# Optimization experiments

Hardware: AMD Instinct MI355X
Metric: run time of the kernel (lower is better)

Reference implementation:

```python
import jax, jax.numpy as jnp
import numpy as np

H, KV, DH = 16, 4, 64  # num_heads, num_kv_heads, head_dim


def setup_inputs() -> dict:
    key = jax.random.key(0)
    k1, k2, k3, k4, k5 = jax.random.split(key, 5)
    B, L, D = 1, 4096, 1024
    s = 0.02
    return {
        "x": jax.random.normal(k1, (B, L, D), dtype=jnp.float32),
        "Wq": jax.random.normal(k2, (D, H * DH), dtype=jnp.float32) * s,
        "Wk": jax.random.normal(k3, (D, KV * DH), dtype=jnp.float32) * s,
        "Wv": jax.random.normal(k4, (D, KV * DH), dtype=jnp.float32) * s,
        "Wo": jax.random.normal(k5, (H * DH, D), dtype=jnp.float32) * s,
    }


def _rotate_half(t):
    t1, t2 = t[..., : DH // 2], t[..., DH // 2 :]
    return jnp.concatenate([-t2, t1], axis=-1)


def reference(x, Wq, Wk, Wv, Wo):
    B, L, D = x.shape
    G = H // KV  # query heads per kv head
    q = (x @ Wq).reshape(B, L, H, DH)
    k = (x @ Wk).reshape(B, L, KV, DH)
    v = (x @ Wv).reshape(B, L, KV, DH)

    # RoPE: inv_freq over even dims, angles duplicated across both halves
    inv_freq = 1.0 / (10000.0 ** (jnp.arange(0, DH, 2, dtype=jnp.float32) / DH))
    t = jnp.arange(L, dtype=jnp.float32)
    freqs = t[:, None] * inv_freq[None, :]                 # [L, DH/2]
    emb = jnp.concatenate([freqs, freqs], axis=-1)[None, :, None, :]  # [1,L,1,DH]
    cos, sin = jnp.cos(emb), jnp.sin(emb)
    q = q * cos + _rotate_half(q) * sin
    k = k * cos + _rotate_half(k) * sin

    # GQA: query head h attends with kv head h // G (repeat_interleave layout)
    qg = q.reshape(B, L, KV, G, DH)
    scale = DH ** -0.5
    attn = jnp.einsum("bqkgd,bskd->bkgqs", qg, k) * scale  # [B,KV,G,L,L]
    attn = jax.nn.softmax(attn, axis=-1)
    out = jnp.einsum("bkgqs,bskd->bqkgd", attn, v).reshape(B, L, H * DH)
    return out @ Wo
```

## Files before the change

kernel.cpp:

```cpp
#include <hip/hip_runtime.h>
#include <math.h>

#define L 4096
#define D 1024
#define H 16
#define KV 4
#define DH 64

typedef __attribute__((ext_vector_type(8))) short bf16x8;
typedef __attribute__((ext_vector_type(4))) float f32x4;

static __device__ __forceinline__ unsigned short f2bf(float f) {
    unsigned u = __float_as_uint(f);
    u = (u + 0x7FFF + ((u >> 16) & 1)) >> 16;
    return (unsigned short)u;
}

#define EXP2F(x) __builtin_amdgcn_exp2f(x)

#define GLD16(src, dst) \
    __builtin_amdgcn_global_load_lds((__attribute__((address_space(1))) void*)(src), \
                                     (__attribute__((address_space(3))) void*)(dst), 16, 0, 0)

__global__ __launch_bounds__(256) void prep_kernel(
        const float* __restrict__ x,  const float* __restrict__ Wq,
        const float* __restrict__ Wk, const float* __restrict__ Wv,
        const float* __restrict__ Wo,
        unsigned short* __restrict__ xb, unsigned short* __restrict__ WqkvT,
        unsigned short* __restrict__ WoT) {
    const int b = blockIdx.x, tid = threadIdx.x;
    if (b < 4096) {
        int i = (b * 256 + tid) * 4;
        float4 v = *(const float4*)&x[i];
        ushort4 o;
        o.x = f2bf(v.x); o.y = f2bf(v.y); o.z = f2bf(v.z); o.w = f2bf(v.w);
        *(ushort4*)&xb[i] = o;
        return;
    }
    __shared__ float t[32][33];
    const float* src; unsigned short* dst; int N, n0, k0;
    if (b < 5120)      { int tq = b - 4096; src = Wq; dst = WqkvT;                     N = 1024; n0 = (tq & 31) * 32; k0 = (tq >> 5) * 32; }
    else if (b < 5376) { int tq = b - 5120; src = Wk; dst = WqkvT + (size_t)1024*1024; N = 256;  n0 = (tq & 7)  * 32; k0 = (tq >> 3) * 32; }
    else if (b < 5632) { int tq = b - 5376; src = Wv; dst = WqkvT + (size_t)1280*1024; N = 256;  n0 = (tq & 7)  * 32; k0 = (tq >> 3) * 32; }
    else               { int tq = b - 5632; src = Wo; dst = WoT;                       N = 1024; n0 = (tq & 31) * 32; k0 = (tq >> 5) * 32; }
    const int tx = tid & 31, ty = tid >> 5;
    #pragma unroll
    for (int j = 0; j < 4; ++j)
        t[ty + 8 * j][tx] = src[(size_t)(k0 + ty + 8 * j) * N + n0 + tx];
    __syncthreads();
    #pragma unroll
    for (int j = 0; j < 4; ++j)
        dst[(size_t)(n0 + ty + 8 * j) * 1024 + k0 + tx] = f2bf(t[tx][ty + 8 * j]);
}

__global__ __launch_bounds__(256) void gemm_bf16(const unsigned short* __restrict__ A,
                                                 const unsigned short* __restrict__ BT,
                                                 float* __restrict__ C,
                                                 int M, int N, int K) {
    __shared__ unsigned short As[128 * 32];
    __shared__ unsigned short Bs[128 * 32];

    const int tid  = threadIdx.x;
    const int w    = tid >> 6;
    const int lane = tid & 63;
    const int c    = lane & 15;
    const int quad = lane >> 4;
    const int wy = w >> 1, wx = w & 1;
    const int row0 = blockIdx.y * 128;
    const int col0 = blockIdx.x * 128;

    const int ld_row = w * 16 + (lane >> 2);
    const int ld_col = (lane & 3) * 8;

    f32x4 acc[4][4];
    #pragma unroll
    for (int mt = 0; mt < 4; ++mt)
        #pragma unroll
        for (int nt = 0; nt < 4; ++nt)
            acc[mt][nt] = (f32x4){0.f, 0.f, 0.f, 0.f};

    for (int k0 = 0; k0 < K; k0 += 32) {
        __syncthreads();
        GLD16(&A [(size_t)(row0 + ld_row)      * K + k0 + ld_col], &As[w * 512]);
        GLD16(&A [(size_t)(row0 + ld_row + 64) * K + k0 + ld_col], &As[w * 512 + 2048]);
        GLD16(&BT[(size_t)(col0 + ld_row)      * K + k0 + ld_col], &Bs[w * 512]);
        GLD16(&BT[(size_t)(col0 + ld_row + 64) * K + k0 + ld_col], &Bs[w * 512 + 2048]);
        __syncthreads();

        bf16x8 af[4], bfr[4];
        #pragma unroll
        for (int mt = 0; mt < 4; ++mt)
            af[mt] = *(const bf16x8*)&As[(wy * 64 + mt * 16 + c) * 32 + quad * 8];
        #pragma unroll
        for (int nt = 0; nt < 4; ++nt)
            bfr[nt] = *(const bf16x8*)&Bs[(wx * 64 + nt * 16 + c) * 32 + quad * 8];

        #pragma unroll
        for (int mt = 0; mt < 4; ++mt)
            #pragma unroll
            for (int nt = 0; nt < 4; ++nt)
                acc[mt][nt] = __builtin_amdgcn_mfma_f32_16x16x32_bf16(af[mt], bfr[nt], acc[mt][nt], 0, 0, 0);
    }

    #pragma unroll
    for (int mt = 0; mt < 4; ++mt)
        #pragma unroll
        for (int nt = 0; nt < 4; ++nt)
            #pragma unroll
            for (int r = 0; r < 4; ++r)
                C[(size_t)(row0 + wy * 64 + mt * 16 + quad * 4 + r) * N
                  + col0 + wx * 64 + nt * 16 + c] = acc[mt][nt][r];
}

__global__ __launch_bounds__(256) void gemm_qkv_rope(
        const unsigned short* __restrict__ A,
        const unsigned short* __restrict__ BT,
        unsigned short* __restrict__ qb,
        unsigned short* __restrict__ kbuf,
        unsigned short* __restrict__ vbuf) {
    __shared__ unsigned short As[128 * 32];
    __shared__ unsigned short Bs[128 * 32];

    const int tid  = threadIdx.x;
    const int w    = tid >> 6;
    const int lane = tid & 63;
    const int c    = lane & 15;
    const int quad = lane >> 4;
    const int wy = w >> 1, wx = w & 1;
    const int row0 = blockIdx.y * 128;
    const int col0 = blockIdx.x * 128;

    const int ld_row = w * 16 + (lane >> 2);
    const int ld_col = (lane & 3) * 8;

    f32x4 acc[4][4];
    #pragma unroll
    for (int mt = 0; mt < 4; ++mt)
        #pragma unroll
        for (int nt = 0; nt < 4; ++nt)
            acc[mt][nt] = (f32x4){0.f, 0.f, 0.f, 0.f};

    for (int k0 = 0; k0 < 1024; k0 += 32) {
        __syncthreads();
        GLD16(&A [(size_t)(row0 + ld_row)      * 1024 + k0 + ld_col], &As[w * 512]);
        GLD16(&A [(size_t)(row0 + ld_row + 64) * 1024 + k0 + ld_col], &As[w * 512 + 2048]);
        GLD16(&BT[(size_t)(col0 + ld_row)      * 1024 + k0 + ld_col], &Bs[w * 512]);
        GLD16(&BT[(size_t)(col0 + ld_row + 64) * 1024 + k0 + ld_col], &Bs[w * 512 + 2048]);
        __syncthreads();

        bf16x8 af[4], bfr[4];
        #pragma unroll
        for (int mt = 0; mt < 4; ++mt)
            af[mt] = *(const bf16x8*)&As[(wy * 64 + mt * 16 + c) * 32 + quad * 8];
        #pragma unroll
        for (int nt = 0; nt < 4; ++nt)
            bfr[nt] = *(const bf16x8*)&Bs[(wx * 64 + nt * 16 + c) * 32 + quad * 8];

        #pragma unroll
        for (int mt = 0; mt < 4; ++mt)
            #pragma unroll
            for (int nt = 0; nt < 4; ++nt)
                acc[mt][nt] = __builtin_amdgcn_mfma_f32_16x16x32_bf16(af[mt], bfr[nt], acc[mt][nt], 0, 0, 0);
    }

    const int colb = col0 + wx * 64;
    if (colb < 1280) {
        unsigned short* dst; int hh, hstride; float scale;
        if (colb < 1024) { dst = qb;   hh = colb >> 6;          hstride = H;  scale = 0.18033688011112042f; }
        else             { dst = kbuf; hh = (colb - 1024) >> 6; hstride = KV; scale = 1.0f; }
        #pragma unroll
        for (int nt = 0; nt < 2; ++nt) {
            int d = nt * 16 + c;
            float invf = EXP2F((float)d * -0.4152410118609203f);
            #pragma unroll
            for (int mt = 0; mt < 4; ++mt)
                #pragma unroll
                for (int r = 0; r < 4; ++r) {
                    int l = row0 + wy * 64 + mt * 16 + quad * 4 + r;
                    float ang = (float)l * invf;
                    float sn = __sinf(ang), cs = __cosf(ang);
                    float x1 = acc[mt][nt][r], x2 = acc[mt][nt + 2][r];
                    dst[((size_t)l * hstride + hh) * DH + d]      = f2bf((x1 * cs - x2 * sn) * scale);
                    dst[((size_t)l * hstride + hh) * DH + d + 32] = f2bf((x2 * cs + x1 * sn) * scale);
                }
        }
    } else {
        int vh = (colb - 1280) >> 6;
        #pragma unroll
        for (int mt = 0; mt < 4; ++mt)
            #pragma unroll
            for (int nt = 0; nt < 4; ++nt)
                #pragma unroll
                for (int r = 0; r < 4; ++r) {
                    int l = row0 + wy * 64 + mt * 16 + quad * 4 + r;
                    vbuf[((size_t)l * KV + vh) * DH + nt * 16 + c] = f2bf(acc[mt][nt][r]);
                }
    }
}

__global__ __launch_bounds__(512, 2) void attn_mfma_kernel(
        const unsigned short* __restrict__ qb,
        const unsigned short* __restrict__ kb,
        const unsigned short* __restrict__ vb,
        unsigned short* __restrict__ ob) {
    __shared__ __align__(16) unsigned short Vt[2][2][64][64];
    __shared__ __align__(16) unsigned short Ps[8][64][64];

    const int tid  = threadIdx.x;
    const int w    = tid >> 6;
    const int lane = tid & 63;
    const int c    = lane & 15;
    const int quad = lane >> 4;
    const int g    = w >> 2;
    const int kv = blockIdx.y;
    const int h  = kv * 4 + (w & 3);
    const int q0 = blockIdx.x * 64;
    const int s_base = g * 2048;

    bf16x8 qfrag[4][2];
    #pragma unroll
    for (int qt = 0; qt < 4; ++qt)
        #pragma unroll
        for (int kt = 0; kt < 2; ++kt)
            qfrag[qt][kt] = *(const bf16x8*)&qb[((size_t)(q0 + qt * 16 + c) * H + h) * DH
                                                + kt * 32 + quad * 8];

    f32x4 oacc[4][4];
    f32x4 oones[4];
    #pragma unroll
    for (int qt = 0; qt < 4; ++qt) {
        oones[qt] = (f32x4){0.f, 0.f, 0.f, 0.f};
        #pragma unroll
        for (int dt = 0; dt < 4; ++dt)
            oacc[qt][dt] = (f32x4){0.f, 0.f, 0.f, 0.f};
    }
    const short one_bf = (short)0x3F80;
    const bf16x8 ones8 = {one_bf, one_bf, one_bf, one_bf, one_bf, one_bf, one_bf, one_bf};

    const int tid8 = tid & 255;
    const int sp = tid8 & 31, dc = tid8 >> 5;
    unsigned short* PsW = &Ps[w][0][0];
    const int xr = c & 7;

    int4 vreg0 = *(const int4*)&vb[((size_t)(s_base + 2 * sp)     * KV + kv) * DH + dc * 8];
    int4 vreg1 = *(const int4*)&vb[((size_t)(s_base + 2 * sp + 1) * KV + kv) * DH + dc * 8];
    bf16x8 kA[4][2], kB[4][2];
    #pragma unroll
    for (int mt = 0; mt < 4; ++mt)
        #pragma unroll
        for (int kt = 0; kt < 2; ++kt)
            kA[mt][kt] = *(const bf16x8*)&kb[((size_t)(s_base + mt * 16 + c) * KV + kv) * DH + kt * 32 + quad * 8];

    auto step = [&](int it, int buf, bf16x8 kc[4][2], bf16x8 kn[4][2]) {
        {
            const unsigned* pa = (const unsigned*)&vreg0;
            const unsigned* pb = (const unsigned*)&vreg1;
            #pragma unroll
            for (int t = 0; t < 4; ++t) {
                unsigned lo = __builtin_amdgcn_perm(pb[t], pa[t], 0x05040100u);
                unsigned hi = __builtin_amdgcn_perm(pb[t], pa[t], 0x07060302u);
                int dl = dc * 8 + 2 * t, dh = dl + 1;
                *(unsigned*)&Vt[g][buf][dl][(((sp >> 2) ^ (dl & 7)) << 3) + 2 * (sp & 3)] = lo;
                *(unsigned*)&Vt[g][buf][dh][(((sp >> 2) ^ (dh & 7)) << 3) + 2 * (sp & 3)] = hi;
            }
        }
        __syncthreads();

        int s1 = s_base + ((it + 1) & 31) * 64;
        vreg0 = *(const int4*)&vb[((size_t)(s1 + 2 * sp)     * KV + kv) * DH + dc * 8];
        vreg1 = *(const int4*)&vb[((size_t)(s1 + 2 * sp + 1) * KV + kv) * DH + dc * 8];
        #pragma unroll
        for (int mt = 0; mt < 4; ++mt)
            #pragma unroll
            for (int kt = 0; kt < 2; ++kt)
                kn[mt][kt] = *(const bf16x8*)&kb[((size_t)(s1 + mt * 16 + c) * KV + kv) * DH + kt * 32 + quad * 8];

        #pragma unroll
        for (int mt = 0; mt < 4; ++mt) {
            f32x4 st[4];
            #pragma unroll
            for (int qt = 0; qt < 4; ++qt) {
                f32x4 a = (f32x4){0.f, 0.f, 0.f, 0.f};
                a = __builtin_amdgcn_mfma_f32_16x16x32_bf16(kc[mt][0], qfrag[qt][0], a, 0, 0, 0);
                a = __builtin_amdgcn_mfma_f32_16x16x32_bf16(kc[mt][1], qfrag[qt][1], a, 0, 0, 0);
                st[qt] = a;
            }
            #pragma unroll
            for (int qt = 0; qt < 4; ++qt) {
                float p0 = EXP2F(st[qt][0]);
                float p1 = EXP2F(st[qt][1]);
                float p2 = EXP2F(st[qt][2]);
                float p3 = EXP2F(st[qt][3]);
                uint2 pk;
                pk.x = __builtin_amdgcn_perm(__float_as_uint(p1), __float_as_uint(p0), 0x07060302u);
                pk.y = __builtin_amdgcn_perm(__float_as_uint(p3), __float_as_uint(p2), 0x07060302u);
                *(uint2*)&PsW[(qt * 16 + c) * 64 + (((2 * mt + (quad >> 1)) ^ xr) << 3) + (quad & 1) * 4] = pk;
            }
        }

        bf16x8 pf[4][2];
        #pragma unroll
        for (int qt = 0; qt < 4; ++qt)
            #pragma unroll
            for (int kt = 0; kt < 2; ++kt)
                pf[qt][kt] = *(const bf16x8*)&PsW[(qt * 16 + c) * 64 + (((kt * 4 + quad) ^ xr) << 3)];

        #pragma unroll
        for (int dt = 0; dt < 4; ++dt) {
            bf16x8 vf0 = *(const bf16x8*)&Vt[g][buf][dt * 16 + c][((0 * 4 + quad) ^ xr) << 3];
            bf16x8 vf1 = *(const bf16x8*)&Vt[g][buf][dt * 16 + c][((1 * 4 + quad) ^ xr) << 3];
            #pragma unroll
            for (int qt = 0; qt < 4; ++qt) {
                oacc[qt][dt] = __builtin_amdgcn_mfma_f32_16x16x32_bf16(pf[qt][0], vf0, oacc[qt][dt], 0, 0, 0);
                oacc[qt][dt] = __builtin_amdgcn_mfma_f32_16x16x32_bf16(pf[qt][1], vf1, oacc[qt][dt], 0, 0, 0);
            }
        }
        #pragma unroll
        for (int qt = 0; qt < 4; ++qt) {
            oones[qt] = __builtin_amdgcn_mfma_f32_16x16x32_bf16(pf[qt][0], ones8, oones[qt], 0, 0, 0);
            oones[qt] = __builtin_amdgcn_mfma_f32_16x16x32_bf16(pf[qt][1], ones8, oones[qt], 0, 0, 0);
        }
    };

    for (int it = 0; it < 32; it += 2) {
        step(it,     0, kA, kB);
        step(it + 1, 1, kB, kA);
    }

    __syncthreads();
    if (g == 1) {
        float* dsto = (float*)&Ps[0][0][0] + (size_t)(w - 4) * 4096 + lane * 64;
        #pragma unroll
        for (int qt = 0; qt < 4; ++qt)
            #pragma unroll
            for (int dt = 0; dt < 4; ++dt)
                *(f32x4*)&dsto[qt * 16 + dt * 4] = oacc[qt][dt];
        float* dsts = (float*)&Vt[0][0][0][0] + (size_t)(w - 4) * 1024 + lane * 16;
        #pragma unroll
        for (int qt = 0; qt < 4; ++qt)
            *(f32x4*)&dsts[qt * 4] = oones[qt];
    }
    __syncthreads();
    if (g == 0) {
        const float* srco = (const float*)&Ps[0][0][0] + (size_t)w * 4096 + lane * 64;
        const float* srcs = (const float*)&Vt[0][0][0][0] + (size_t)w * 1024 + lane * 16;
        #pragma unroll
        for (int qt = 0; qt < 4; ++qt) {
            f32x4 po = *(const f32x4*)&srcs[qt * 4];
            oones[qt] += po;
            #pragma unroll
            for (int dt = 0; dt < 4; ++dt)
                oacc[qt][dt] += *(const f32x4*)&srco[qt * 16 + dt * 4];
        }
        #pragma unroll
        for (int qt = 0; qt < 4; ++qt)
            #pragma unroll
            for (int r = 0; r < 4; ++r) {
                float inv = 1.0f / oones[qt][r];
                int row = q0 + qt * 16 + quad * 4 + r;
                #pragma unroll
                for (int dt = 0; dt < 4; ++dt)
                    ob[(size_t)row * (H * DH) + h * DH + dt * 16 + c] = f2bf(oacc[qt][dt][r] * inv);
            }
    }
}

extern "C" void kernel_launch(void* const* d_in, const int* in_sizes, int n_in,
                              void* d_out, int out_size, void* d_ws, size_t ws_size,
                              hipStream_t stream) {
    const float* x  = (const float*)d_in[0];
    const float* Wq = (const float*)d_in[1];
    const float* Wk = (const float*)d_in[2];
    const float* Wv = (const float*)d_in[3];
    const float* Wo = (const float*)d_in[4];
    float* out = (float*)d_out;

    char* ws = (char*)d_ws;
    unsigned short* xb    = (unsigned short*)ws;
    unsigned short* ob    = xb;
    unsigned short* qb    = (unsigned short*)(ws + 8388608);
    unsigned short* kb    = (unsigned short*)(ws + 16777216);
    unsigned short* vb    = (unsigned short*)(ws + 18874368);
    unsigned short* WqkvT = (unsigned short*)(ws + 20971520);
    unsigned short* WoT   = (unsigned short*)(ws + 24117248);

    dim3 blk(256);

    prep_kernel<<<6656, blk, 0, stream>>>(x, Wq, Wk, Wv, Wo, xb, WqkvT, WoT);

    gemm_qkv_rope<<<dim3(12, 32), blk, 0, stream>>>(xb, WqkvT, qb, kb, vb);

    attn_mfma_kernel<<<dim3(L / 64, KV), dim3(512), 0, stream>>>(qb, kb, vb, ob);

    gemm_bf16<<<dim3(D / 128, L / 128), blk, 0, stream>>>(ob, WoT, out, L, D, D);
}
```

Baseline: 230.4 us.

## Store V transposed from QKV GEMM and load V fragments directly in attention

The QKV GEMM epilogue now writes V in a transposed [kv*64+d][L] layout with packed 8-byte stores. The attention kernel then loads V MFMA operands straight from global memory instead of staging and transposing V through LDS. This drops the per-iteration __syncthreads and the LDS V buffer, and shrinks shared memory to one buffer. The final cross-group reduction is redone in two halves through that smaller LDS region. The cost is more global and L2 traffic per wave, since each wave group reloads V with no sharing through LDS.

```diff
diff --git a/kernel.cpp b/kernel.cpp
--- a/kernel.cpp
+++ b/kernel.cpp
@@ -117,7 +117,7 @@
         const unsigned short* __restrict__ BT,
         unsigned short* __restrict__ qb,
         unsigned short* __restrict__ kbuf,
-        unsigned short* __restrict__ vbuf) {
+        unsigned short* __restrict__ vtb) {
     __shared__ unsigned short As[128 * 32];
     __shared__ unsigned short Bs[128 * 32];
 
@@ -187,24 +187,25 @@
     } else {
         int vh = (colb - 1280) >> 6;
         #pragma unroll
-        for (int mt = 0; mt < 4; ++mt)
-            #pragma unroll
-            for (int nt = 0; nt < 4; ++nt)
-                #pragma unroll
-                for (int r = 0; r < 4; ++r) {
-                    int l = row0 + wy * 64 + mt * 16 + quad * 4 + r;
-                    vbuf[((size_t)l * KV + vh) * DH + nt * 16 + c] = f2bf(acc[mt][nt][r]);
-                }
+        for (int mt = 0; mt < 4; ++mt) {
+            int l0 = row0 + wy * 64 + mt * 16 + quad * 4;
+            #pragma unroll
+            for (int nt = 0; nt < 4; ++nt) {
+                unsigned u0 = (unsigned)f2bf(acc[mt][nt][0]) | ((unsigned)f2bf(acc[mt][nt][1]) << 16);
+                unsigned u1 = (unsigned)f2bf(acc[mt][nt][2]) | ((unsigned)f2bf(acc[mt][nt][3]) << 16);
+                uint2 pk; pk.x = u0; pk.y = u1;
+                *(uint2*)&vtb[(size_t)((vh * 64 + nt * 16 + c) << 12) + l0] = pk;
+            }
+        }
     }
 }
 
 __global__ __launch_bounds__(512, 2) void attn_mfma_kernel(
         const unsigned short* __restrict__ qb,
         const unsigned short* __restrict__ kb,
-        const unsigned short* __restrict__ vb,
+        const unsigned short* __restrict__ vtb,
         unsigned short* __restrict__ ob) {
-    __shared__ __align__(16) unsigned short Vt[2][2][64][64];
-    __shared__ __align__(16) unsigned short Ps[8][64][64];
+    __shared__ __align__(16) unsigned short lds[32768];
 
     const int tid  = threadIdx.x;
     const int w    = tid >> 6;
@@ -237,13 +238,10 @@
     const short one_bf = (short)0x3F80;
     const bf16x8 ones8 = {one_bf, one_bf, one_bf, one_bf, one_bf, one_bf, one_bf, one_bf};
 
-    const int tid8 = tid & 255;
-    const int sp = tid8 & 31, dc = tid8 >> 5;
-    unsigned short* PsW = &Ps[w][0][0];
+    unsigned short* PsW = &lds[w * 4096];
     const int xr = c & 7;
-
-    int4 vreg0 = *(const int4*)&vb[((size_t)(s_base + 2 * sp)     * KV + kv) * DH + dc * 8];
-    int4 vreg1 = *(const int4*)&vb[((size_t)(s_base + 2 * sp + 1) * KV + kv) * DH + dc * 8];
+    const unsigned short* vrow = &vtb[(size_t)((kv * 64 + c) << 12)];
+
     bf16x8 kA[4][2], kB[4][2];
     #pragma unroll
     for (int mt = 0; mt < 4; ++mt)
@@ -251,24 +249,17 @@
         for (int kt = 0; kt < 2; ++kt)
             kA[mt][kt] = *(const bf16x8*)&kb[((size_t)(s_base + mt * 16 + c) * KV + kv) * DH + kt * 32 + quad * 8];
 
-    auto step = [&](int it, int buf, bf16x8 kc[4][2], bf16x8 kn[4][2]) {
-        {
-            const unsigned* pa = (const unsigned*)&vreg0;
-            const unsigned* pb = (const unsigned*)&vreg1;
-            #pragma unroll
-            for (int t = 0; t < 4; ++t) {
-                unsigned lo = __builtin_amdgcn_perm(pb[t], pa[t], 0x05040100u);
-                unsigned hi = __builtin_amdgcn_perm(pb[t], pa[t], 0x07060302u);
-                int dl = dc * 8 + 2 * t, dh = dl + 1;
-                *(unsigned*)&Vt[g][buf][dl][(((sp >> 2) ^ (dl & 7)) << 3) + 2 * (sp & 3)] = lo;
-                *(unsigned*)&Vt[g][buf][dh][(((sp >> 2) ^ (dh & 7)) << 3) + 2 * (sp & 3)] = hi;
-            }
-        }
-        __syncthreads();
-
-        int s1 = s_base + ((it + 1) & 31) * 64;
-        vreg0 = *(const int4*)&vb[((size_t)(s1 + 2 * sp)     * KV + kv) * DH + dc * 8];
-        vreg1 = *(const int4*)&vb[((size_t)(s1 + 2 * sp + 1) * KV + kv) * DH + dc * 8];
+    auto step = [&](int it, bf16x8 kc[4][2], bf16x8 kn[4][2]) {
+        const int s_cur = s_base + it * 64;
+
+        bf16x8 vf[4][2];
+        #pragma unroll
+        for (int dt = 0; dt < 4; ++dt)
+            #pragma unroll
+            for (int kt = 0; kt < 2; ++kt)
+                vf[dt][kt] = *(const bf16x8*)&vrow[(size_t)(dt * 16 << 12) + s_cur + kt * 32 + quad * 8];
+
+        const int s1 = s_base + ((it + 1) & 31) * 64;
         #pragma unroll
         for (int mt = 0; mt < 4; ++mt)
             #pragma unroll
@@ -306,15 +297,12 @@
                 pf[qt][kt] = *(const bf16x8*)&PsW[(qt * 16 + c) * 64 + (((kt * 4 + quad) ^ xr) << 3)];
 
         #pragma unroll
-        for (int dt = 0; dt < 4; ++dt) {
-            bf16x8 vf0 = *(const bf16x8*)&Vt[g][buf][dt * 16 + c][((0 * 4 + quad) ^ xr) << 3];
-            bf16x8 vf1 = *(const bf16x8*)&Vt[g][buf][dt * 16 + c][((1 * 4 + quad) ^ xr) << 3];
+        for (int dt = 0; dt < 4; ++dt)
             #pragma unroll
             for (int qt = 0; qt < 4; ++qt) {
-                oacc[qt][dt] = __builtin_amdgcn_mfma_f32_16x16x32_bf16(pf[qt][0], vf0, oacc[qt][dt], 0, 0, 0);
-                oacc[qt][dt] = __builtin_amdgcn_mfma_f32_16x16x32_bf16(pf[qt][1], vf1, oacc[qt][dt], 0, 0, 0);
-            }
-        }
+                oacc[qt][dt] = __builtin_amdgcn_mfma_f32_16x16x32_bf16(pf[qt][0], vf[dt][0], oacc[qt][dt], 0, 0, 0);
+                oacc[qt][dt] = __builtin_amdgcn_mfma_f32_16x16x32_bf16(pf[qt][1], vf[dt][1], oacc[qt][dt], 0, 0, 0);
+            }
         #pragma unroll
         for (int qt = 0; qt < 4; ++qt) {
             oones[qt] = __builtin_amdgcn_mfma_f32_16x16x32_bf16(pf[qt][0], ones8, oones[qt], 0, 0, 0);
@@ -323,35 +311,49 @@
     };
 
     for (int it = 0; it < 32; it += 2) {
-        step(it,     0, kA, kB);
-        step(it + 1, 1, kB, kA);
-    }
-
+        step(it,     kA, kB);
+        step(it + 1, kB, kA);
+    }
+
+    float* dump = (float*)lds;
     __syncthreads();
-    if (g == 1) {
-        float* dsto = (float*)&Ps[0][0][0] + (size_t)(w - 4) * 4096 + lane * 64;
-        #pragma unroll
-        for (int qt = 0; qt < 4; ++qt)
-            #pragma unroll
-            for (int dt = 0; dt < 4; ++dt)
-                *(f32x4*)&dsto[qt * 16 + dt * 4] = oacc[qt][dt];
-        float* dsts = (float*)&Vt[0][0][0][0] + (size_t)(w - 4) * 1024 + lane * 16;
-        #pragma unroll
-        for (int qt = 0; qt < 4; ++qt)
-            *(f32x4*)&dsts[qt * 4] = oones[qt];
-    }
-    __syncthreads();
+    #pragma unroll
+    for (int half = 0; half < 2; ++half) {
+        if (g == 1) {
+            int slot = (w - 4) * 64 + lane;
+            #pragma unroll
+            for (int q2 = 0; q2 < 2; ++q2) {
+                int qt = half * 2 + q2;
+                #pragma unroll
+                for (int dt = 0; dt < 4; ++dt)
+                    #pragma unroll
+                    for (int r = 0; r < 4; ++r)
+                        dump[(q2 * 16 + dt * 4 + r) * 256 + slot] = oacc[qt][dt][r];
+                #pragma unroll
+                for (int r = 0; r < 4; ++r)
+                    dump[(32 + q2 * 4 + r) * 256 + slot] = oones[qt][r];
+            }
+        }
+        __syncthreads();
+        if (g == 0) {
+            int slot = w * 64 + lane;
+            #pragma unroll
+            for (int q2 = 0; q2 < 2; ++q2) {
+                int qt = half * 2 + q2;
+                #pragma unroll
+                for (int dt = 0; dt < 4; ++dt)
+                    #pragma unroll
+                    for (int r = 0; r < 4; ++r)
+                        oacc[qt][dt][r] += dump[(q2 * 16 + dt * 4 + r) * 256 + slot];
+                #pragma unroll
+                for (int r = 0; r < 4; ++r)
+                    oones[qt][r] += dump[(32 + q2 * 4 + r) * 256 + slot];
+            }
+        }
+        __syncthreads();
+    }
+
     if (g == 0) {
-        const float* srco = (const float*)&Ps[0][0][0] + (size_t)w * 4096 + lane * 64;
-        const float* srcs = (const float*)&Vt[0][0][0][0] + (size_t)w * 1024 + lane * 16;
-        #pragma unroll
-        for (int qt = 0; qt < 4; ++qt) {
-            f32x4 po = *(const f32x4*)&srcs[qt * 4];
-            oones[qt] += po;
-            #pragma unroll
-            for (int dt = 0; dt < 4; ++dt)
-                oacc[qt][dt] += *(const f32x4*)&srco[qt * 16 + dt * 4];
-        }
         #pragma unroll
         for (int qt = 0; qt < 4; ++qt)
             #pragma unroll
@@ -380,7 +382,7 @@
     unsigned short* ob    = xb;
     unsigned short* qb    = (unsigned short*)(ws + 8388608);
     unsigned short* kb    = (unsigned short*)(ws + 16777216);
-    unsigned short* vb    = (unsigned short*)(ws + 18874368);
+    unsigned short* vtb   = (unsigned short*)(ws + 18874368);
     unsigned short* WqkvT = (unsigned short*)(ws + 20971520);
     unsigned short* WoT   = (unsigned short*)(ws + 24117248);
 
@@ -388,9 +390,9 @@
 
     prep_kernel<<<6656, blk, 0, stream>>>(x, Wq, Wk, Wv, Wo, xb, WqkvT, WoT);
 
-    gemm_qkv_rope<<<dim3(12, 32), blk, 0, stream>>>(xb, WqkvT, qb, kb, vb);
-
-    attn_mfma_kernel<<<dim3(L / 64, KV), dim3(512), 0, stream>>>(qb, kb, vb, ob);
+    gemm_qkv_rope<<<dim3(12, 32), blk, 0, stream>>>(xb, WqkvT, qb, kb, vtb);
+
+    attn_mfma_kernel<<<dim3(L / 64, KV), dim3(512), 0, stream>>>(qb, kb, vtb, ob);
 
     gemm_bf16<<<dim3(D / 128, L / 128), blk, 0, stream>>>(ob, WoT, out, L, D, D);
 }
```

Result: slower. 255.2 us (+10.7%).
